# Kernel optimization log

Hardware: AMD Instinct MI355X
Metric: run time of the kernel (lower is better)

## Reference

```python
import jax, jax.numpy as jnp
import numpy as np

N_NODES = 40962
N_EDGES = 245760
K = 10  # gaussian kernels
D = 2   # pseudo-coordinate dim
EPS = 1e-15


def gmm_conv(x, edge_index, pseudo, g, mu, sigma, root, bias):
    """PyG GMMConv with aggr='mean', root_weight=True.
    x: [N, Cin], edge_index: [2, E] (row 0 = source j, row 1 = target i),
    pseudo: [E, D], g: [Cin, K*Cout], mu/sigma: [K, D], root: [Cin, Cout], bias: [Cout].
    """
    src, dst = edge_index[0], edge_index[1]
    E = pseudo.shape[0]
    # Gaussian mixture edge weights: [E, K]
    diff = pseudo[:, None, :] - mu[None, :, :]                     # [E, K, D]
    w = jnp.exp(jnp.sum(-0.5 * diff * diff / (EPS + sigma[None] ** 2), axis=-1))
    xj = x[src]                                                    # [E, Cin] gather
    y = (xj @ g).reshape(E, K, -1)                                 # [E, K, Cout]
    msg = jnp.sum(y * w[:, :, None], axis=1)                       # [E, Cout]
    agg = jax.ops.segment_sum(msg, dst, num_segments=N_NODES)      # scatter-add
    deg = jax.ops.segment_sum(jnp.ones((E,), x.dtype), dst, num_segments=N_NODES)
    agg = agg / jnp.maximum(deg, 1.0)[:, None]                     # mean aggregation
    return agg + x @ root + bias


def setup_inputs() -> dict:
    key = jax.random.key(0)
    ks = jax.random.split(key, 20)
    Cin, Ch, Cout = 64, 64, 128
    sc = lambda fan: 1.0 / np.sqrt(fan)
    inp = {
        "x": jax.random.normal(ks[0], (N_NODES, Cin), jnp.float32),
        "edge_index": jax.random.randint(ks[1], (2, N_EDGES), 0, N_NODES, jnp.int32),
        "pseudo": jax.random.uniform(ks[2], (N_EDGES, D), jnp.float32),
        # conv1: Cin -> Ch
        "g1": jax.random.normal(ks[3], (Cin, K * Ch), jnp.float32) * sc(Cin),
        "mu1": jax.random.uniform(ks[4], (K, D), jnp.float32),
        "sigma1": jax.random.uniform(ks[5], (K, D), jnp.float32) + 0.5,
        "root1": jax.random.normal(ks[6], (Cin, Ch), jnp.float32) * sc(Cin),
        "b1": jnp.zeros((Ch,), jnp.float32),
        # conv2: Ch -> Cout
        "g2": jax.random.normal(ks[7], (Ch, K * Cout), jnp.float32) * sc(Ch),
        "mu2": jax.random.uniform(ks[8], (K, D), jnp.float32),
        "sigma2": jax.random.uniform(ks[9], (K, D), jnp.float32) + 0.5,
        "root2": jax.random.normal(ks[10], (Ch, Cout), jnp.float32) * sc(Ch),
        "b2": jnp.zeros((Cout,), jnp.float32),
        # shortcut: Cin -> Cout (size_in != size_out)
        "gs": jax.random.normal(ks[11], (Cin, K * Cout), jnp.float32) * sc(Cin),
        "mus": jax.random.uniform(ks[12], (K, D), jnp.float32),
        "sigmas": jax.random.uniform(ks[13], (K, D), jnp.float32) + 0.5,
        "roots": jax.random.normal(ks[14], (Cin, Cout), jnp.float32) * sc(Cin),
        "bs": jnp.zeros((Cout,), jnp.float32),
    }
    return inp


def reference(x, edge_index, pseudo, g1, mu1, sigma1, root1, b1,
              g2, mu2, sigma2, root2, b2, gs, mus, sigmas, roots, bs):
    h = gmm_conv(x, edge_index, pseudo, g1, mu1, sigma1, root1, b1)
    h = jax.nn.relu(h)
    y = gmm_conv(h, edge_index, pseudo, g2, mu2, sigma2, root2, b2)
    x_s = gmm_conv(x, edge_index, pseudo, gs, mus, sigmas, roots, bs)
    return jax.nn.relu(y + x_s)
```

## Files before the change

### kernel.cpp

```cpp
#include <hip/hip_runtime.h>
#include <hip/hip_bf16.h>

using bf16 = __hip_bfloat16;
typedef __attribute__((ext_vector_type(8))) short short8;
typedef __attribute__((ext_vector_type(4))) float float4v;

#define N_NODES 40962
#define N_EDGES 245760
#define NP      41024
#define KG      10
#define SCAN_B  256
#define NBLK    ((NP + SCAN_B - 1) / SCAN_B)
#define GRID1   (NP / 64)

#define CVT_V   (N_NODES * 64 / 8)
#define CVT_BLK ((CVT_V + 255) / 256)
#define W3_BLK  (N_EDGES / 256)
#define PACK_N  (64 * 704 + 2 * 128 * 704)
#define PACK_BLK (PACK_N / 256)


__device__ __forceinline__ float ldf(const void* p, size_t i, int isf32) {
    return isf32 ? ((const float*)p)[i] : __bfloat162float(((const bf16*)p)[i]);
}
__device__ __forceinline__ float blo(unsigned u) { return __uint_as_float(u << 16); }
__device__ __forceinline__ float bhi(unsigned u) { return __uint_as_float(u & 0xffff0000u); }
__device__ __forceinline__ unsigned pk2(float a, float b) {
    union { bf16 h[2]; unsigned u; } t;
    t.h[0] = __float2bfloat16(a);
    t.h[1] = __float2bfloat16(b);
    return t.u;
}
__device__ __forceinline__ int rfl(int v) { return __builtin_amdgcn_readfirstlane(v); }

__device__ __forceinline__ void gll16(const void* g, void* l) {
    __builtin_amdgcn_global_load_lds(
        (const __attribute__((address_space(1))) void*)g,
        (__attribute__((address_space(3))) void*)l, 16, 0, 0);
}

__global__ void k_detect_count(const void* x, const int* __restrict__ ei,
                               int* __restrict__ flag, int* __restrict__ deg) {
    if (blockIdx.x == 0) {
        __shared__ int huge_c, zero_even;
        if (threadIdx.x == 0) { huge_c = 0; zero_even = 0; }
        __syncthreads();
        const bf16* xb = (const bf16*)x;
        int lh = 0, lz = 0;
        for (int i = threadIdx.x; i < 8192; i += 256) {
            float v = __bfloat162float(xb[i]);
            if (!(fabsf(v) <= 1e4f)) lh++;
            if ((i & 1) == 0 && v == 0.0f) lz++;
        }
        atomicAdd(&huge_c, lh);
        atomicAdd(&zero_even, lz);
        __syncthreads();
        if (threadIdx.x == 0) flag[0] = (huge_c > 0 || zero_even > 3000) ? 1 : 0;
    } else {
        int e = (blockIdx.x - 1) * 256 + threadIdx.x;
        if (e < N_EDGES) atomicAdd(&deg[ei[N_EDGES + e]], 1);
    }
}

__global__ void k_scan1(const int* __restrict__ deg, int* __restrict__ offs,
                        int* __restrict__ bsum) {
    __shared__ int buf[SCAN_B];
    int t = threadIdx.x, b = blockIdx.x;
    int i = b * SCAN_B + t;
    int v = (i < NP) ? deg[i] : 0;
    buf[t] = v;
    __syncthreads();
    for (int off = 1; off < SCAN_B; off <<= 1) {
        int a = (t >= off) ? buf[t - off] : 0;
        __syncthreads();
        buf[t] += a;
        __syncthreads();
    }
    if (i < NP) offs[i] = buf[t] - v;
    if (t == SCAN_B - 1) bsum[b] = buf[t];
}

__global__ void k_scan3m(int* __restrict__ offs, const int* __restrict__ bsum,
                         const int* __restrict__ deg, int* __restrict__ cur,
                         float* __restrict__ invdeg) {
    __shared__ int buf[256];
    int t = threadIdx.x, b = blockIdx.x;
    int v = (t < NBLK) ? bsum[t] : 0;
    buf[t] = v;
    __syncthreads();
    for (int off = 1; off < 256; off <<= 1) {
        int a = (t >= off) ? buf[t - off] : 0;
        __syncthreads();
        buf[t] += a;
        __syncthreads();
    }
    int bofs = (b > 0) ? buf[b - 1] : 0;
    int total = buf[NBLK - 1];
    int i = b * 256 + t;
    if (i < NP) {
        int o = offs[i] + bofs;
        offs[i] = o;
        cur[i] = o;
        int d = deg[i];
        invdeg[i] = 1.0f / (float)(d > 1 ? d : 1);
    }
    if (i == 0) offs[NP] = total;
}

__global__ void k_fill(const int* __restrict__ ei, int* __restrict__ cur,
                       int* __restrict__ ep, int* __restrict__ csr_src) {
    int e = blockIdx.x * 256 + threadIdx.x;
    if (e < N_EDGES) {
        int pos = atomicAdd(&cur[ei[N_EDGES + e]], 1);
        ep[e] = pos;
        csr_src[pos] = ei[e];
    }
}

__device__ __forceinline__ void gw_one(float p0, float p1, const void* mu,
                                       const void* sg, int f, float* out) {
#pragma unroll
    for (int k = 0; k < KG; k++) {
        float m0 = ldf(mu, 2 * k + 0, f), m1 = ldf(mu, 2 * k + 1, f);
        float s0 = ldf(sg, 2 * k + 0, f), s1 = ldf(sg, 2 * k + 1, f);
        float d0 = p0 - m0, d1 = p1 - m1;
        float t = -0.5f * (d0 * d0 / (1e-15f + s0 * s0) + d1 * d1 / (1e-15f + s1 * s1));
        out[k] = __expf(t);
    }
}

__device__ __forceinline__ void pack_frag(const void* g, const void* root, int f,
                                          int idx, int Cout, bf16* Bp) {
    int j = idx & 7;
    int lane = (idx >> 3) & 63;
    int rem = idx >> 9;
    int kc = rem % 22;
    int n = rem / 22;
    int col = n * 16 + (lane & 15);
    int k = kc * 32 + (lane >> 4) * 8 + j;
    float v;
    if (k < 512) {
        int cin = k >> 3, kg = k & 7;
        v = ldf(g, (size_t)cin * (KG * Cout) + (size_t)kg * Cout + col, f);
    } else if (k < 640) {
        int jj = k - 512;
        int cin = jj >> 1, kg = 8 + (jj & 1);
        v = ldf(g, (size_t)cin * (KG * Cout) + (size_t)kg * Cout + col, f);
    } else {
        v = ldf(root, (size_t)(k - 640) * Cout + col, f);
    }
    Bp[idx] = __float2bfloat16(v);
}

__global__ void k_prep_all(const void* __restrict__ x, const void* __restrict__ pseudo,
                           const void* mu1, const void* sg1, const void* mu2,
                           const void* sg2, const void* mus, const void* sgs,
                           const void* g1, const void* root1, const void* g2,
                           const void* root2, const void* gs, const void* roots,
                           const int* __restrict__ flag, const int* __restrict__ ep,
                           bf16* __restrict__ Xf, bf16* __restrict__ wcab,
                           bf16* __restrict__ wc2, bf16* wt1p, bf16* wt2p,
                           bf16* wtsp) {
    int b = blockIdx.x;
    int tid = threadIdx.x;
    int f = flag[0];
    if (b < CVT_BLK) {
        int i = b * 256 + tid;
        if (i < CVT_V) {
            int node = i >> 3, j = i & 7;
            uint4 u;
            if (f) {
                const float4* xf = (const float4*)x;
                float4 a = xf[2 * i], c = xf[2 * i + 1];
                union { bf16 t[8]; uint4 u; } tt;
                tt.t[0] = __float2bfloat16(a.x); tt.t[1] = __float2bfloat16(a.y);
                tt.t[2] = __float2bfloat16(a.z); tt.t[3] = __float2bfloat16(a.w);
                tt.t[4] = __float2bfloat16(c.x); tt.t[5] = __float2bfloat16(c.y);
                tt.t[6] = __float2bfloat16(c.z); tt.t[7] = __float2bfloat16(c.w);
                u = tt.u;
            } else {
                u = ((const uint4*)x)[i];
            }
            *(uint4*)(Xf + ((size_t)(j >> 2) * NP + node) * 32 + (j & 3) * 8) = u;
        }
    } else if (b < CVT_BLK + W3_BLK) {
        int e = (b - CVT_BLK) * 256 + tid;
        float p0 = ldf(pseudo, (size_t)e * 2 + 0, f);
        float p1 = ldf(pseudo, (size_t)e * 2 + 1, f);
        float o1[KG], o2[KG], os[KG];
        gw_one(p0, p1, mu1, sg1, f, o1);
        gw_one(p0, p1, mu2, sg2, f, o2);
        gw_one(p0, p1, mus, sgs, f, os);
        int pos = ep[e];
        unsigned* d = (unsigned*)wcab + (size_t)pos * 10;
        d[0] = pk2(o1[0], o1[1]); d[1] = pk2(o1[2], o1[3]);
        d[2] = pk2(o1[4], o1[5]); d[3] = pk2(o1[6], o1[7]);
        d[4] = pk2(o1[8], o1[9]);
        d[5] = pk2(os[0], os[1]); d[6] = pk2(os[2], os[3]);
        d[7] = pk2(os[4], os[5]); d[8] = pk2(os[6], os[7]);
        d[9] = pk2(os[8], os[9]);
        unsigned* d2 = (unsigned*)wc2 + (size_t)pos * 5;
        d2[0] = pk2(o2[0], o2[1]); d2[1] = pk2(o2[2], o2[3]);
        d2[2] = pk2(o2[4], o2[5]); d2[3] = pk2(o2[6], o2[7]);
        d2[4] = pk2(o2[8], o2[9]);
    } else {
        int idx = (b - CVT_BLK - W3_BLK) * 256 + tid;
        if (idx < 64 * 704) {
            pack_frag(g1, root1, f, idx, 64, wt1p);
        } else if (idx < 64 * 704 + 128 * 704) {
            pack_frag(g2, root2, f, idx - 64 * 704, 128, wt2p);
        } else {
            pack_frag(gs, roots, f, idx - 64 * 704 - 128 * 704, 128, wtsp);
        }
    }
}

__device__ __forceinline__ void store_zf(bf16* Zf, int wid, int lane, const float* a,
                                         float inv) {
    union { bf16 h[8]; uint4 u; } p;
#pragma unroll
    for (int k = 0; k < 8; k++) p.h[k] = __float2bfloat16(a[k] * inv);
    *(uint4*)(Zf + ((size_t)(lane >> 2) * NP + wid) * 32 + (lane & 3) * 8) = p.u;
    *(unsigned*)(Zf + ((size_t)(16 + (lane >> 4)) * NP + wid) * 32 + (lane & 15) * 2) =
        pk2(a[8] * inv, a[9] * inv);
}

__device__ __forceinline__ float ldx_frag(const bf16* X, int src, int lane) {
    return __bfloat162float(X[((size_t)(lane >> 5) * NP + src) * 32 + (lane & 31)]);
}

__device__ __forceinline__ int clampe(int idx) {
    return idx > N_EDGES - 1 ? N_EDGES - 1 : idx;
}

__global__ void k_gather2(const int* __restrict__ offs, const int* __restrict__ csr_src,
                          const bf16* __restrict__ wcab,
                          const float* __restrict__ invdeg, const bf16* __restrict__ X,
                          bf16* __restrict__ Za, bf16* __restrict__ Zb) {
    int wid = (blockIdx.x * 256 + threadIdx.x) >> 6;
    int lane = threadIdx.x & 63;
    if (wid >= NP) return;
    float aa[KG], ab[KG];
#pragma unroll
    for (int k = 0; k < KG; k++) { aa[k] = 0.0f; ab[k] = 0.0f; }
    int beg = rfl(offs[wid]);
    int end = rfl(offs[wid + 1]);
    int cnt = end - beg;
    const unsigned* wb = (const unsigned*)wcab;

    int s0 = rfl(csr_src[clampe(beg + 0)]);
    int s1 = rfl(csr_src[clampe(beg + 1)]);
    int sC = rfl(csr_src[clampe(beg + 2)]);
    float xv0 = ldx_frag(X, s0, lane);
    float xv1 = ldx_frag(X, s1, lane);
    const unsigned* wp0 = wb + (size_t)clampe(beg + 0) * 10;
    unsigned c0 = wp0[0], c1 = wp0[1], c2 = wp0[2], c3 = wp0[3], c4 = wp0[4];
    unsigned c5 = wp0[5], c6 = wp0[6], c7 = wp0[7], c8 = wp0[8], c9 = wp0[9];
    const unsigned* wp1 = wb + (size_t)clampe(beg + 1) * 10;
    unsigned n0 = wp1[0], n1 = wp1[1], n2 = wp1[2], n3 = wp1[3], n4 = wp1[4];
    unsigned n5 = wp1[5], n6 = wp1[6], n7 = wp1[7], n8 = wp1[8], n9 = wp1[9];

    for (int t = 0; t < cnt; ++t) {
        int sN = rfl(csr_src[clampe(beg + t + 3)]);
        float xv2 = ldx_frag(X, sC, lane);
        const unsigned* wp2 = wb + (size_t)clampe(beg + t + 2) * 10;
        unsigned m0 = wp2[0], m1 = wp2[1], m2 = wp2[2], m3 = wp2[3], m4 = wp2[4];
        unsigned m5 = wp2[5], m6 = wp2[6], m7 = wp2[7], m8 = wp2[8], m9 = wp2[9];
        aa[0] += blo(c0) * xv0; aa[1] += bhi(c0) * xv0;
        aa[2] += blo(c1) * xv0; aa[3] += bhi(c1) * xv0;
        aa[4] += blo(c2) * xv0; aa[5] += bhi(c2) * xv0;
        aa[6] += blo(c3) * xv0; aa[7] += bhi(c3) * xv0;
        aa[8] += blo(c4) * xv0; aa[9] += bhi(c4) * xv0;
        ab[0] += blo(c5) * xv0; ab[1] += bhi(c5) * xv0;
        ab[2] += blo(c6) * xv0; ab[3] += bhi(c6) * xv0;
        ab[4] += blo(c7) * xv0; ab[5] += bhi(c7) * xv0;
        ab[6] += blo(c8) * xv0; ab[7] += bhi(c8) * xv0;
        ab[8] += blo(c9) * xv0; ab[9] += bhi(c9) * xv0;
        xv0 = xv1; xv1 = xv2; sC = sN;
        c0 = n0; c1 = n1; c2 = n2; c3 = n3; c4 = n4;
        c5 = n5; c6 = n6; c7 = n7; c8 = n8; c9 = n9;
        n0 = m0; n1 = m1; n2 = m2; n3 = m3; n4 = m4;
        n5 = m5; n6 = m6; n7 = m7; n8 = m8; n9 = m9;
    }
    float inv = invdeg[wid];
    store_zf(Za, wid, lane, aa, inv);
    store_zf(Zb, wid, lane, ab, inv);
}

__global__ void k_gather(const int* __restrict__ offs, const int* __restrict__ csr_src,
                         const bf16* __restrict__ w, int wstride,
                         const float* __restrict__ invdeg,
                         const bf16* __restrict__ X, bf16* __restrict__ Z) {
    int wid = (blockIdx.x * 256 + threadIdx.x) >> 6;
    int lane = threadIdx.x & 63;
    if (wid >= NP) return;
    float acc[KG];
#pragma unroll
    for (int k = 0; k < KG; k++) acc[k] = 0.0f;
    int beg = rfl(offs[wid]);
    int end = rfl(offs[wid + 1]);
    int cnt = end - beg;

    int s0 = rfl(csr_src[clampe(beg + 0)]);
    int s1 = rfl(csr_src[clampe(beg + 1)]);
    int sC = rfl(csr_src[clampe(beg + 2)]);
    float xv0 = ldx_frag(X, s0, lane);
    float xv1 = ldx_frag(X, s1, lane);
    const unsigned* wp0 = (const unsigned*)(w + (size_t)clampe(beg + 0) * wstride);
    unsigned c0 = wp0[0], c1 = wp0[1], c2 = wp0[2], c3 = wp0[3], c4 = wp0[4];
    const unsigned* wp1 = (const unsigned*)(w + (size_t)clampe(beg + 1) * wstride);
    unsigned n0 = wp1[0], n1 = wp1[1], n2 = wp1[2], n3 = wp1[3], n4 = wp1[4];

    for (int t = 0; t < cnt; ++t) {
        int sN = rfl(csr_src[clampe(beg + t + 3)]);
        float xv2 = ldx_frag(X, sC, lane);
        const unsigned* wp2 = (const unsigned*)(w + (size_t)clampe(beg + t + 2) * wstride);
        unsigned m0 = wp2[0], m1 = wp2[1], m2 = wp2[2], m3 = wp2[3], m4 = wp2[4];
        acc[0] += blo(c0) * xv0; acc[1] += bhi(c0) * xv0;
        acc[2] += blo(c1) * xv0; acc[3] += bhi(c1) * xv0;
        acc[4] += blo(c2) * xv0; acc[5] += bhi(c2) * xv0;
        acc[6] += blo(c3) * xv0; acc[7] += bhi(c3) * xv0;
        acc[8] += blo(c4) * xv0; acc[9] += bhi(c4) * xv0;
        xv0 = xv1; xv1 = xv2; sC = sN;
        c0 = n0; c1 = n1; c2 = n2; c3 = n3; c4 = n4;
        n0 = m0; n1 = m1; n2 = m2; n3 = m3; n4 = m4;
    }
    store_zf(Z, wid, lane, acc, invdeg[wid]);
}

template <int NT, int MODE>
__device__ __forceinline__ void gemm_body(
    int bid, const bf16* __restrict__ Zf, const bf16* __restrict__ Xf,
    const bf16* __restrict__ Bp, const void* __restrict__ bias, int f,
    const bf16* __restrict__ addsrc, bf16* __restrict__ outb,
    void* __restrict__ outp, bf16* __restrict__ sB) {
    constexpr int Cout = NT * 16;
    int lane = threadIdx.x & 63;
    int wave = threadIdx.x >> 6;
    int m = lane & 15, quad = lane >> 4;
    int row0 = bid * 64 + wave * 16;

    const bf16* arow = Zf + ((size_t)(row0 + m)) * 32 + quad * 8;
    const bf16* xrow = Xf + ((size_t)(row0 + m)) * 32 + quad * 8;

    float4v acc[NT];
#pragma unroll
    for (int n = 0; n < NT; n++) acc[n] = (float4v){0.f, 0.f, 0.f, 0.f};

#pragma unroll
    for (int n = wave; n < NT; n += 4)
        gll16(Bp + ((size_t)(n * 22 + 0) * 64 + lane) * 8, sB + n * 512);
    short8 a_cur = *(const short8*)arow;
    __syncthreads();

#pragma unroll
    for (int kc = 0; kc < 22; kc++) {
        int buf = kc & 1;
        short8 a_nxt;
        if (kc < 21) {
            int kn = kc + 1;
#pragma unroll
            for (int n = wave; n < NT; n += 4)
                gll16(Bp + ((size_t)(n * 22 + kn) * 64 + lane) * 8,
                      sB + (size_t)(1 - buf) * NT * 512 + n * 512);
            a_nxt = (kn < 20)
                ? *(const short8*)(arow + (size_t)kn * NP * 32)
                : *(const short8*)(xrow + (size_t)(kn - 20) * NP * 32);
        }
        const bf16* bb = sB + (size_t)buf * NT * 512 + lane * 8;
#pragma unroll
        for (int n = 0; n < NT; n++) {
            short8 b = *(const short8*)(bb + (size_t)n * 512);
            acc[n] = __builtin_amdgcn_mfma_f32_16x16x32_bf16(a_cur, b, acc[n], 0, 0, 0);
        }
        __syncthreads();
        if (kc < 21) a_cur = a_nxt;
    }

#pragma unroll
    for (int n = 0; n < NT; n++) {
        int gcol = n * 16 + m;
        float bv = ldf(bias, gcol, f);
#pragma unroll
        for (int r = 0; r < 4; r++) {
            int grow = row0 + quad * 4 + r;
            if (grow >= N_NODES) continue;
            float v = acc[n][r] + bv;
            if (MODE == 0) {
                outb[((size_t)(gcol >> 5) * NP + grow) * 32 + (gcol & 31)] =
                    __float2bfloat16(fmaxf(v, 0.f));
            } else if (MODE == 1) {
                outb[(size_t)grow * Cout + gcol] = __float2bfloat16(v);
            } else {
                size_t oidx = (size_t)grow * Cout + gcol;
                v = fmaxf(v + __bfloat162float(addsrc[oidx]), 0.f);
                if (f) ((float*)outp)[oidx] = v;
                else   ((bf16*)outp)[oidx] = __float2bfloat16(v);
            }
        }
    }
}

__global__ __launch_bounds__(256) void k_gemm_pair(
    const bf16* __restrict__ za, const bf16* __restrict__ zb,
    const bf16* __restrict__ Xf, const bf16* __restrict__ wt1p,
    const bf16* __restrict__ wtsp, const void* __restrict__ b1,
    const void* __restrict__ bs, const int* __restrict__ flag,
    bf16* __restrict__ hf, bf16* __restrict__ ys) {
    __shared__ bf16 sB[2 * 8 * 512];
    int f = flag[0];
    if (blockIdx.x < GRID1)
        gemm_body<4, 0>(blockIdx.x, za, Xf, wt1p, b1, f, nullptr, hf, nullptr, sB);
    else
        gemm_body<8, 1>(blockIdx.x - GRID1, zb, Xf, wtsp, bs, f, nullptr, ys, nullptr,
                        sB);
}

template <int NT, int MODE>
__global__ __launch_bounds__(256) void k_gemm_one(
    const bf16* __restrict__ Zf, const bf16* __restrict__ Xf,
    const bf16* __restrict__ Bp, const void* __restrict__ bias,
    const int* __restrict__ flag, const bf16* __restrict__ addsrc,
    bf16* __restrict__ outb, void* __restrict__ outp) {
    __shared__ bf16 sB[2 * NT * 512];
    gemm_body<NT, MODE>(blockIdx.x, Zf, Xf, Bp, bias, flag[0], addsrc, outb, outp, sB);
}

extern "C" void kernel_launch(void* const* d_in, const int* in_sizes, int n_in,
                              void* d_out, int out_size, void* d_ws, size_t ws_size,
                              hipStream_t stream) {
    const void* x      = d_in[0];
    const int*  ei     = (const int*)d_in[1];
    const void* pseudo = d_in[2];
    const void* g1     = d_in[3];
    const void* mu1    = d_in[4];
    const void* sg1    = d_in[5];
    const void* root1  = d_in[6];
    const void* b1     = d_in[7];
    const void* g2     = d_in[8];
    const void* mu2    = d_in[9];
    const void* sg2    = d_in[10];
    const void* root2  = d_in[11];
    const void* b2     = d_in[12];
    const void* gs     = d_in[13];
    const void* mus    = d_in[14];
    const void* sgs    = d_in[15];
    const void* roots  = d_in[16];
    const void* bs     = d_in[17];

    char* ws = (char*)d_ws;
    size_t off = 0;
    auto alloc = [&](size_t bytes) -> char* {
        char* p = ws + off;
        off += (bytes + 255) & ~(size_t)255;
        return p;
    };
    const size_t ZSZ = (size_t)20 * NP * 32 * 2;
    const size_t XFS = (size_t)2 * NP * 32 * 2;

    int*   flag   = (int*)alloc(256);
    int*   deg    = (int*)alloc((size_t)NP * 4);
    int*   offs   = (int*)alloc((size_t)(NP + 1) * 4);
    int*   cur    = (int*)alloc((size_t)NP * 4);
    float* invdeg = (float*)alloc((size_t)NP * 4);
    int*   bsum   = (int*)alloc((size_t)NBLK * 4);
    int*   ep     = (int*)alloc((size_t)N_EDGES * 4);
    int*   csrs   = (int*)alloc((size_t)N_EDGES * 4);
    bf16*  Xf     = (bf16*)alloc(XFS);
    bf16*  hf     = (bf16*)alloc(XFS);
    bf16*  ys     = (bf16*)alloc((size_t)N_NODES * 128 * 2);
    bf16*  wt1p   = (bf16*)alloc((size_t)64 * 704 * 2);
    bf16*  wt2p   = (bf16*)alloc((size_t)128 * 704 * 2);
    bf16*  wtsp   = (bf16*)alloc((size_t)128 * 704 * 2);
    bf16*  wcab   = (bf16*)alloc((size_t)N_EDGES * 20 * 2);
    bf16*  wc2    = (bf16*)alloc((size_t)N_EDGES * 10 * 2);
    size_t common_end = off;

    bf16* za = (bf16*)alloc(ZSZ);
    bf16* zb = (bf16*)alloc(ZSZ);
    bool big = (off <= ws_size);

    hipMemsetAsync(deg, 0, (size_t)NP * 4, stream);
    k_detect_count<<<1 + (N_EDGES + 255) / 256, 256, 0, stream>>>(x, ei, flag, deg);
    k_scan1<<<NBLK, SCAN_B, 0, stream>>>(deg, offs, bsum);
    k_scan3m<<<NBLK, 256, 0, stream>>>(offs, bsum, deg, cur, invdeg);
    k_fill<<<(N_EDGES + 255) / 256, 256, 0, stream>>>(ei, cur, ep, csrs);
    k_prep_all<<<CVT_BLK + W3_BLK + PACK_BLK, 256, 0, stream>>>(
        x, pseudo, mu1, sg1, mu2, sg2, mus, sgs, g1, root1, g2, root2, gs, roots,
        flag, ep, Xf, wcab, wc2, wt1p, wt2p, wtsp);

    if (big) {
        k_gather2<<<NP / 4, 256, 0, stream>>>(offs, csrs, wcab, invdeg, Xf, za, zb);
        k_gemm_pair<<<2 * GRID1, 256, 0, stream>>>(za, zb, Xf, wt1p, wtsp, b1, bs,
                                                   flag, hf, ys);
        k_gather<<<NP / 4, 256, 0, stream>>>(offs, csrs, wc2, 10, invdeg, hf, za);
        k_gemm_one<8, 2><<<GRID1, 256, 0, stream>>>(za, hf, wt2p, b2, flag, ys,
                                                    (bf16*)nullptr, d_out);
    } else {
        off = common_end;
        bf16* z = (bf16*)alloc(ZSZ);
        k_gather<<<NP / 4, 256, 0, stream>>>(offs, csrs, wcab, 20, invdeg, Xf, z);
        k_gemm_one<4, 0><<<GRID1, 256, 0, stream>>>(z, Xf, wt1p, b1, flag,
                                                    (const bf16*)nullptr, hf, nullptr);
        k_gather<<<NP / 4, 256, 0, stream>>>(offs, csrs, wcab + 10, 20, invdeg, Xf, z);
        k_gemm_one<8, 1><<<GRID1, 256, 0, stream>>>(z, Xf, wtsp, bs, flag,
                                                    (const bf16*)nullptr, ys, nullptr);
        k_gather<<<NP / 4, 256, 0, stream>>>(offs, csrs, wc2, 10, invdeg, hf, z);
        k_gemm_one<8, 2><<<GRID1, 256, 0, stream>>>(z, hf, wt2p, b2, flag, ys,
                                                    (bf16*)nullptr, d_out);
    }
}
```

Before: 267.7 us.

## Fuse edge gather with MFMA GEMM through LDS, merging shortcut into conv2

Replaces the separate gather kernels (which wrote large Z intermediates to global memory) and GEMM kernels with two fused kernels. Each block gathers 16 nodes into an LDS tile, then runs MFMA directly from LDS. The second kernel computes conv2 and the shortcut conv together and accumulates both into one result, so the ys intermediate and the final add pass go away. This cuts global traffic and launch count. In exchange, per-block GEMM tiles are small, B fragments are read straight from global without LDS staging, and the shortcut gather now happens after conv1 instead of alongside it.

```diff
diff --git a/kernel.cpp b/kernel.cpp
--- a/kernel.cpp
+++ b/kernel.cpp
@@ -11,7 +11,7 @@
 #define KG      10
 #define SCAN_B  256
 #define NBLK    ((NP + SCAN_B - 1) / SCAN_B)
-#define GRID1   (NP / 64)
+#define GRIDF   (NP / 16)
 
 #define CVT_V   (N_NODES * 64 / 8)
 #define CVT_BLK ((CVT_V + 255) / 256)
@@ -19,6 +19,9 @@
 #define PACK_N  (64 * 704 + 2 * 128 * 704)
 #define PACK_BLK (PACK_N / 256)
 
+#define ZRS  40
+#define ZKS  648
+#define ZSZE 12960
 
 __device__ __forceinline__ float ldf(const void* p, size_t i, int isf32) {
     return isf32 ? ((const float*)p)[i] : __bfloat162float(((const bf16*)p)[i]);
@@ -32,12 +35,6 @@
     return t.u;
 }
 __device__ __forceinline__ int rfl(int v) { return __builtin_amdgcn_readfirstlane(v); }
-
-__device__ __forceinline__ void gll16(const void* g, void* l) {
-    __builtin_amdgcn_global_load_lds(
-        (const __attribute__((address_space(1))) void*)g,
-        (__attribute__((address_space(3))) void*)l, 16, 0, 0);
-}
 
 __global__ void k_detect_count(const void* x, const int* __restrict__ ei,
                                int* __restrict__ flag, int* __restrict__ deg) {
@@ -158,9 +155,9 @@
                            const void* g1, const void* root1, const void* g2,
                            const void* root2, const void* gs, const void* roots,
                            const int* __restrict__ flag, const int* __restrict__ ep,
-                           bf16* __restrict__ Xf, bf16* __restrict__ wcab,
-                           bf16* __restrict__ wc2, bf16* wt1p, bf16* wt2p,
-                           bf16* wtsp) {
+                           bf16* __restrict__ Xf, bf16* __restrict__ wc1,
+                           bf16* __restrict__ wcs, bf16* __restrict__ wc2,
+                           bf16* wt1p, bf16* wt2p, bf16* wtsp) {
     int b = blockIdx.x;
     int tid = threadIdx.x;
     int f = flag[0];
@@ -192,13 +189,14 @@
         gw_one(p0, p1, mu2, sg2, f, o2);
         gw_one(p0, p1, mus, sgs, f, os);
         int pos = ep[e];
-        unsigned* d = (unsigned*)wcab + (size_t)pos * 10;
-        d[0] = pk2(o1[0], o1[1]); d[1] = pk2(o1[2], o1[3]);
-        d[2] = pk2(o1[4], o1[5]); d[3] = pk2(o1[6], o1[7]);
-        d[4] = pk2(o1[8], o1[9]);
-        d[5] = pk2(os[0], os[1]); d[6] = pk2(os[2], os[3]);
-        d[7] = pk2(os[4], os[5]); d[8] = pk2(os[6], os[7]);
-        d[9] = pk2(os[8], os[9]);
+        unsigned* d1 = (unsigned*)wc1 + (size_t)pos * 5;
+        d1[0] = pk2(o1[0], o1[1]); d1[1] = pk2(o1[2], o1[3]);
+        d1[2] = pk2(o1[4], o1[5]); d1[3] = pk2(o1[6], o1[7]);
+        d1[4] = pk2(o1[8], o1[9]);
+        unsigned* ds = (unsigned*)wcs + (size_t)pos * 5;
+        ds[0] = pk2(os[0], os[1]); ds[1] = pk2(os[2], os[3]);
+        ds[2] = pk2(os[4], os[5]); ds[3] = pk2(os[6], os[7]);
+        ds[4] = pk2(os[8], os[9]);
         unsigned* d2 = (unsigned*)wc2 + (size_t)pos * 5;
         d2[0] = pk2(o2[0], o2[1]); d2[1] = pk2(o2[2], o2[3]);
         d2[2] = pk2(o2[4], o2[5]); d2[3] = pk2(o2[6], o2[7]);
@@ -215,16 +213,6 @@
     }
 }
 
-__device__ __forceinline__ void store_zf(bf16* Zf, int wid, int lane, const float* a,
-                                         float inv) {
-    union { bf16 h[8]; uint4 u; } p;
-#pragma unroll
-    for (int k = 0; k < 8; k++) p.h[k] = __float2bfloat16(a[k] * inv);
-    *(uint4*)(Zf + ((size_t)(lane >> 2) * NP + wid) * 32 + (lane & 3) * 8) = p.u;
-    *(unsigned*)(Zf + ((size_t)(16 + (lane >> 4)) * NP + wid) * 32 + (lane & 15) * 2) =
-        pk2(a[8] * inv, a[9] * inv);
-}
-
 __device__ __forceinline__ float ldx_frag(const bf16* X, int src, int lane) {
     return __bfloat162float(X[((size_t)(lane >> 5) * NP + src) * 32 + (lane & 31)]);
 }
@@ -233,197 +221,194 @@
     return idx > N_EDGES - 1 ? N_EDGES - 1 : idx;
 }
 
-__global__ void k_gather2(const int* __restrict__ offs, const int* __restrict__ csr_src,
-                          const bf16* __restrict__ wcab,
-                          const float* __restrict__ invdeg, const bf16* __restrict__ X,
-                          bf16* __restrict__ Za, bf16* __restrict__ Zb) {
-    int wid = (blockIdx.x * 256 + threadIdx.x) >> 6;
-    int lane = threadIdx.x & 63;
-    if (wid >= NP) return;
-    float aa[KG], ab[KG];
-#pragma unroll
-    for (int k = 0; k < KG; k++) { aa[k] = 0.0f; ab[k] = 0.0f; }
-    int beg = rfl(offs[wid]);
-    int end = rfl(offs[wid + 1]);
-    int cnt = end - beg;
-    const unsigned* wb = (const unsigned*)wcab;
-
-    int s0 = rfl(csr_src[clampe(beg + 0)]);
-    int s1 = rfl(csr_src[clampe(beg + 1)]);
-    int sC = rfl(csr_src[clampe(beg + 2)]);
-    float xv0 = ldx_frag(X, s0, lane);
-    float xv1 = ldx_frag(X, s1, lane);
-    const unsigned* wp0 = wb + (size_t)clampe(beg + 0) * 10;
-    unsigned c0 = wp0[0], c1 = wp0[1], c2 = wp0[2], c3 = wp0[3], c4 = wp0[4];
-    unsigned c5 = wp0[5], c6 = wp0[6], c7 = wp0[7], c8 = wp0[8], c9 = wp0[9];
-    const unsigned* wp1 = wb + (size_t)clampe(beg + 1) * 10;
-    unsigned n0 = wp1[0], n1 = wp1[1], n2 = wp1[2], n3 = wp1[3], n4 = wp1[4];
-    unsigned n5 = wp1[5], n6 = wp1[6], n7 = wp1[7], n8 = wp1[8], n9 = wp1[9];
-
-    for (int t = 0; t < cnt; ++t) {
-        int sN = rfl(csr_src[clampe(beg + t + 3)]);
-        float xv2 = ldx_frag(X, sC, lane);
-        const unsigned* wp2 = wb + (size_t)clampe(beg + t + 2) * 10;
-        unsigned m0 = wp2[0], m1 = wp2[1], m2 = wp2[2], m3 = wp2[3], m4 = wp2[4];
-        unsigned m5 = wp2[5], m6 = wp2[6], m7 = wp2[7], m8 = wp2[8], m9 = wp2[9];
-        aa[0] += blo(c0) * xv0; aa[1] += bhi(c0) * xv0;
-        aa[2] += blo(c1) * xv0; aa[3] += bhi(c1) * xv0;
-        aa[4] += blo(c2) * xv0; aa[5] += bhi(c2) * xv0;
-        aa[6] += blo(c3) * xv0; aa[7] += bhi(c3) * xv0;
-        aa[8] += blo(c4) * xv0; aa[9] += bhi(c4) * xv0;
-        ab[0] += blo(c5) * xv0; ab[1] += bhi(c5) * xv0;
-        ab[2] += blo(c6) * xv0; ab[3] += bhi(c6) * xv0;
-        ab[4] += blo(c7) * xv0; ab[5] += bhi(c7) * xv0;
-        ab[6] += blo(c8) * xv0; ab[7] += bhi(c8) * xv0;
-        ab[8] += blo(c9) * xv0; ab[9] += bhi(c9) * xv0;
-        xv0 = xv1; xv1 = xv2; sC = sN;
-        c0 = n0; c1 = n1; c2 = n2; c3 = n3; c4 = n4;
-        c5 = n5; c6 = n6; c7 = n7; c8 = n8; c9 = n9;
-        n0 = m0; n1 = m1; n2 = m2; n3 = m3; n4 = m4;
-        n5 = m5; n6 = m6; n7 = m7; n8 = m8; n9 = m9;
-    }
-    float inv = invdeg[wid];
-    store_zf(Za, wid, lane, aa, inv);
-    store_zf(Zb, wid, lane, ab, inv);
-}
-
-__global__ void k_gather(const int* __restrict__ offs, const int* __restrict__ csr_src,
-                         const bf16* __restrict__ w, int wstride,
-                         const float* __restrict__ invdeg,
-                         const bf16* __restrict__ X, bf16* __restrict__ Z) {
-    int wid = (blockIdx.x * 256 + threadIdx.x) >> 6;
-    int lane = threadIdx.x & 63;
-    if (wid >= NP) return;
-    float acc[KG];
-#pragma unroll
-    for (int k = 0; k < KG; k++) acc[k] = 0.0f;
-    int beg = rfl(offs[wid]);
-    int end = rfl(offs[wid + 1]);
-    int cnt = end - beg;
-
-    int s0 = rfl(csr_src[clampe(beg + 0)]);
-    int s1 = rfl(csr_src[clampe(beg + 1)]);
-    int sC = rfl(csr_src[clampe(beg + 2)]);
-    float xv0 = ldx_frag(X, s0, lane);
-    float xv1 = ldx_frag(X, s1, lane);
-    const unsigned* wp0 = (const unsigned*)(w + (size_t)clampe(beg + 0) * wstride);
-    unsigned c0 = wp0[0], c1 = wp0[1], c2 = wp0[2], c3 = wp0[3], c4 = wp0[4];
-    const unsigned* wp1 = (const unsigned*)(w + (size_t)clampe(beg + 1) * wstride);
-    unsigned n0 = wp1[0], n1 = wp1[1], n2 = wp1[2], n3 = wp1[3], n4 = wp1[4];
-
-    for (int t = 0; t < cnt; ++t) {
-        int sN = rfl(csr_src[clampe(beg + t + 3)]);
-        float xv2 = ldx_frag(X, sC, lane);
-        const unsigned* wp2 = (const unsigned*)(w + (size_t)clampe(beg + t + 2) * wstride);
-        unsigned m0 = wp2[0], m1 = wp2[1], m2 = wp2[2], m3 = wp2[3], m4 = wp2[4];
-        acc[0] += blo(c0) * xv0; acc[1] += bhi(c0) * xv0;
-        acc[2] += blo(c1) * xv0; acc[3] += bhi(c1) * xv0;
-        acc[4] += blo(c2) * xv0; acc[5] += bhi(c2) * xv0;
-        acc[6] += blo(c3) * xv0; acc[7] += bhi(c3) * xv0;
-        acc[8] += blo(c4) * xv0; acc[9] += bhi(c4) * xv0;
-        xv0 = xv1; xv1 = xv2; sC = sN;
-        c0 = n0; c1 = n1; c2 = n2; c3 = n3; c4 = n4;
-        n0 = m0; n1 = m1; n2 = m2; n3 = m3; n4 = m4;
-    }
-    store_zf(Z, wid, lane, acc, invdeg[wid]);
-}
-
-template <int NT, int MODE>
-__device__ __forceinline__ void gemm_body(
-    int bid, const bf16* __restrict__ Zf, const bf16* __restrict__ Xf,
-    const bf16* __restrict__ Bp, const void* __restrict__ bias, int f,
-    const bf16* __restrict__ addsrc, bf16* __restrict__ outb,
-    void* __restrict__ outp, bf16* __restrict__ sB) {
-    constexpr int Cout = NT * 16;
+__device__ __forceinline__ void store_zlds(bf16* z, int r, int lane, const float* a,
+                                           float inv) {
+    union { bf16 h[8]; uint4 u; } p;
+#pragma unroll
+    for (int k = 0; k < 8; k++) p.h[k] = __float2bfloat16(a[k] * inv);
+    *(uint4*)(z + (lane >> 2) * ZKS + r * ZRS + (lane & 3) * 8) = p.u;
+    *(unsigned*)(z + (16 + (lane >> 4)) * ZKS + r * ZRS + (lane & 15) * 2) =
+        pk2(a[8] * inv, a[9] * inv);
+}
+
+__global__ __launch_bounds__(256) void k_fused1(
+    const int* __restrict__ offs, const int* __restrict__ csr_src,
+    const bf16* __restrict__ wc1, const float* __restrict__ invdeg,
+    const bf16* __restrict__ Xf, const bf16* __restrict__ wt1p,
+    const void* __restrict__ b1, const int* __restrict__ flag,
+    bf16* __restrict__ hf) {
+    __shared__ bf16 zA[ZSZE];
     int lane = threadIdx.x & 63;
     int wave = threadIdx.x >> 6;
+    int bid = blockIdx.x;
+    const unsigned* wb = (const unsigned*)wc1;
+
+    for (int i = 0; i < 4; i++) {
+        int r = wave * 4 + i;
+        int node = bid * 16 + r;
+        float acc[KG];
+#pragma unroll
+        for (int k = 0; k < KG; k++) acc[k] = 0.0f;
+        int beg = rfl(offs[node]);
+        int end = rfl(offs[node + 1]);
+        int cnt = end - beg;
+        int sC = rfl(csr_src[clampe(beg + 2)]);
+        float xv0 = ldx_frag(Xf, rfl(csr_src[clampe(beg + 0)]), lane);
+        float xv1 = ldx_frag(Xf, rfl(csr_src[clampe(beg + 1)]), lane);
+        const unsigned* wp0 = wb + (size_t)clampe(beg + 0) * 5;
+        unsigned c0 = wp0[0], c1 = wp0[1], c2 = wp0[2], c3 = wp0[3], c4 = wp0[4];
+        const unsigned* wp1 = wb + (size_t)clampe(beg + 1) * 5;
+        unsigned n0 = wp1[0], n1 = wp1[1], n2 = wp1[2], n3 = wp1[3], n4 = wp1[4];
+        for (int t = 0; t < cnt; ++t) {
+            int sN = rfl(csr_src[clampe(beg + t + 3)]);
+            float xv2 = ldx_frag(Xf, sC, lane);
+            const unsigned* wp2 = wb + (size_t)clampe(beg + t + 2) * 5;
+            unsigned m0 = wp2[0], m1 = wp2[1], m2 = wp2[2], m3 = wp2[3], m4 = wp2[4];
+            acc[0] += blo(c0) * xv0; acc[1] += bhi(c0) * xv0;
+            acc[2] += blo(c1) * xv0; acc[3] += bhi(c1) * xv0;
+            acc[4] += blo(c2) * xv0; acc[5] += bhi(c2) * xv0;
+            acc[6] += blo(c3) * xv0; acc[7] += bhi(c3) * xv0;
+            acc[8] += blo(c4) * xv0; acc[9] += bhi(c4) * xv0;
+            xv0 = xv1; xv1 = xv2; sC = sN;
+            c0 = n0; c1 = n1; c2 = n2; c3 = n3; c4 = n4;
+            n0 = m0; n1 = m1; n2 = m2; n3 = m3; n4 = m4;
+        }
+        store_zlds(zA, r, lane, acc, invdeg[node]);
+    }
+    __syncthreads();
+
     int m = lane & 15, quad = lane >> 4;
-    int row0 = bid * 64 + wave * 16;
-
-    const bf16* arow = Zf + ((size_t)(row0 + m)) * 32 + quad * 8;
+    int row0 = bid * 16;
+    float4v acc4 = (float4v){0.f, 0.f, 0.f, 0.f};
+    const bf16* brow = wt1p + ((size_t)(wave * 22) * 64 + lane) * 8;
     const bf16* xrow = Xf + ((size_t)(row0 + m)) * 32 + quad * 8;
-
-    float4v acc[NT];
-#pragma unroll
-    for (int n = 0; n < NT; n++) acc[n] = (float4v){0.f, 0.f, 0.f, 0.f};
-
-#pragma unroll
-    for (int n = wave; n < NT; n += 4)
-        gll16(Bp + ((size_t)(n * 22 + 0) * 64 + lane) * 8, sB + n * 512);
-    short8 a_cur = *(const short8*)arow;
+#pragma unroll
+    for (int kc = 0; kc < 22; kc++) {
+        short8 a = (kc < 20)
+            ? *(const short8*)(zA + kc * ZKS + m * ZRS + quad * 8)
+            : *(const short8*)(xrow + (size_t)(kc - 20) * NP * 32);
+        short8 b = *(const short8*)(brow + (size_t)kc * 512);
+        acc4 = __builtin_amdgcn_mfma_f32_16x16x32_bf16(a, b, acc4, 0, 0, 0);
+    }
+    int f = flag[0];
+    int gcol = wave * 16 + m;
+    float bv = ldf(b1, gcol, f);
+#pragma unroll
+    for (int r = 0; r < 4; r++) {
+        int grow = row0 + quad * 4 + r;
+        if (grow >= N_NODES) continue;
+        float v = fmaxf(acc4[r] + bv, 0.f);
+        hf[((size_t)(gcol >> 5) * NP + grow) * 32 + (gcol & 31)] = __float2bfloat16(v);
+    }
+}
+
+__global__ __launch_bounds__(256) void k_fused2(
+    const int* __restrict__ offs, const int* __restrict__ csr_src,
+    const bf16* __restrict__ wc2, const bf16* __restrict__ wcs,
+    const float* __restrict__ invdeg, const bf16* __restrict__ Xf,
+    const bf16* __restrict__ hf, const bf16* __restrict__ wt2p,
+    const bf16* __restrict__ wtsp, const void* __restrict__ b2,
+    const void* __restrict__ bs, const int* __restrict__ flag,
+    void* __restrict__ out) {
+    __shared__ bf16 z2[ZSZE];
+    __shared__ bf16 zs[ZSZE];
+    int lane = threadIdx.x & 63;
+    int wave = threadIdx.x >> 6;
+    int bid = blockIdx.x;
+    const unsigned* w2b = (const unsigned*)wc2;
+    const unsigned* wsb = (const unsigned*)wcs;
+
+    for (int i = 0; i < 4; i++) {
+        int r = wave * 4 + i;
+        int node = bid * 16 + r;
+        float a2[KG], as[KG];
+#pragma unroll
+        for (int k = 0; k < KG; k++) { a2[k] = 0.0f; as[k] = 0.0f; }
+        int beg = rfl(offs[node]);
+        int end = rfl(offs[node + 1]);
+        int cnt = end - beg;
+        int sC = rfl(csr_src[clampe(beg + 2)]);
+        int s0 = rfl(csr_src[clampe(beg + 0)]);
+        int s1 = rfl(csr_src[clampe(beg + 1)]);
+        float hv0 = ldx_frag(hf, s0, lane), xv0 = ldx_frag(Xf, s0, lane);
+        float hv1 = ldx_frag(hf, s1, lane), xv1 = ldx_frag(Xf, s1, lane);
+        const unsigned* p20 = w2b + (size_t)clampe(beg + 0) * 5;
+        unsigned c0 = p20[0], c1 = p20[1], c2 = p20[2], c3 = p20[3], c4 = p20[4];
+        const unsigned* ps0 = wsb + (size_t)clampe(beg + 0) * 5;
+        unsigned d0 = ps0[0], d1 = ps0[1], d2 = ps0[2], d3 = ps0[3], d4 = ps0[4];
+        const unsigned* p21 = w2b + (size_t)clampe(beg + 1) * 5;
+        unsigned n0 = p21[0], n1 = p21[1], n2 = p21[2], n3 = p21[3], n4 = p21[4];
+        const unsigned* ps1 = wsb + (size_t)clampe(beg + 1) * 5;
+        unsigned o0 = ps1[0], o1 = ps1[1], o2 = ps1[2], o3 = ps1[3], o4 = ps1[4];
+        for (int t = 0; t < cnt; ++t) {
+            int sN = rfl(csr_src[clampe(beg + t + 3)]);
+            float hv2 = ldx_frag(hf, sC, lane);
+            float xv2 = ldx_frag(Xf, sC, lane);
+            const unsigned* p22 = w2b + (size_t)clampe(beg + t + 2) * 5;
+            unsigned m0 = p22[0], m1 = p22[1], m2 = p22[2], m3 = p22[3], m4 = p22[4];
+            const unsigned* ps2 = wsb + (size_t)clampe(beg + t + 2) * 5;
+            unsigned q0 = ps2[0], q1 = ps2[1], q2 = ps2[2], q3 = ps2[3], q4 = ps2[4];
+            a2[0] += blo(c0) * hv0; a2[1] += bhi(c0) * hv0;
+            a2[2] += blo(c1) * hv0; a2[3] += bhi(c1) * hv0;
+            a2[4] += blo(c2) * hv0; a2[5] += bhi(c2) * hv0;
+            a2[6] += blo(c3) * hv0; a2[7] += bhi(c3) * hv0;
+            a2[8] += blo(c4) * hv0; a2[9] += bhi(c4) * hv0;
+            as[0] += blo(d0) * xv0; as[1] += bhi(d0) * xv0;
+            as[2] += blo(d1) * xv0; as[3] += bhi(d1) * xv0;
+            as[4] += blo(d2) * xv0; as[5] += bhi(d2) * xv0;
+            as[6] += blo(d3) * xv0; as[7] += bhi(d3) * xv0;
+            as[8] += blo(d4) * xv0; as[9] += bhi(d4) * xv0;
+            hv0 = hv1; hv1 = hv2; xv0 = xv1; xv1 = xv2; sC = sN;
+            c0 = n0; c1 = n1; c2 = n2; c3 = n3; c4 = n4;
+            n0 = m0; n1 = m1; n2 = m2; n3 = m3; n4 = m4;
+            d0 = o0; d1 = o1; d2 = o2; d3 = o3; d4 = o4;
+            o0 = q0; o1 = q1; o2 = q2; o3 = q3; o4 = q4;
+        }
+        float inv = invdeg[node];
+        store_zlds(z2, r, lane, a2, inv);
+        store_zlds(zs, r, lane, as, inv);
+    }
     __syncthreads();
 
-#pragma unroll
-    for (int kc = 0; kc < 22; kc++) {
-        int buf = kc & 1;
-        short8 a_nxt;
-        if (kc < 21) {
-            int kn = kc + 1;
-#pragma unroll
-            for (int n = wave; n < NT; n += 4)
-                gll16(Bp + ((size_t)(n * 22 + kn) * 64 + lane) * 8,
-                      sB + (size_t)(1 - buf) * NT * 512 + n * 512);
-            a_nxt = (kn < 20)
-                ? *(const short8*)(arow + (size_t)kn * NP * 32)
-                : *(const short8*)(xrow + (size_t)(kn - 20) * NP * 32);
-        }
-        const bf16* bb = sB + (size_t)buf * NT * 512 + lane * 8;
-#pragma unroll
-        for (int n = 0; n < NT; n++) {
-            short8 b = *(const short8*)(bb + (size_t)n * 512);
-            acc[n] = __builtin_amdgcn_mfma_f32_16x16x32_bf16(a_cur, b, acc[n], 0, 0, 0);
-        }
-        __syncthreads();
-        if (kc < 21) a_cur = a_nxt;
-    }
-
-#pragma unroll
-    for (int n = 0; n < NT; n++) {
+    int m = lane & 15, quad = lane >> 4;
+    int row0 = bid * 16;
+    const bf16* hrow = hf + ((size_t)(row0 + m)) * 32 + quad * 8;
+    const bf16* xrow = Xf + ((size_t)(row0 + m)) * 32 + quad * 8;
+    int f = flag[0];
+#pragma unroll
+    for (int tt = 0; tt < 2; tt++) {
+        int n = wave + tt * 4;
+        float4v acc4 = (float4v){0.f, 0.f, 0.f, 0.f};
+        const bf16* b2row = wt2p + ((size_t)(n * 22) * 64 + lane) * 8;
+        const bf16* bsrow = wtsp + ((size_t)(n * 22) * 64 + lane) * 8;
+#pragma unroll
+        for (int kc = 0; kc < 22; kc++) {
+            short8 a = (kc < 20)
+                ? *(const short8*)(z2 + kc * ZKS + m * ZRS + quad * 8)
+                : *(const short8*)(hrow + (size_t)(kc - 20) * NP * 32);
+            short8 b = *(const short8*)(b2row + (size_t)kc * 512);
+            acc4 = __builtin_amdgcn_mfma_f32_16x16x32_bf16(a, b, acc4, 0, 0, 0);
+        }
+#pragma unroll
+        for (int kc = 0; kc < 22; kc++) {
+            short8 a = (kc < 20)
+                ? *(const short8*)(zs + kc * ZKS + m * ZRS + quad * 8)
+                : *(const short8*)(xrow + (size_t)(kc - 20) * NP * 32);
+            short8 b = *(const short8*)(bsrow + (size_t)kc * 512);
+            acc4 = __builtin_amdgcn_mfma_f32_16x16x32_bf16(a, b, acc4, 0, 0, 0);
+        }
         int gcol = n * 16 + m;
-        float bv = ldf(bias, gcol, f);
+        float bv = ldf(b2, gcol, f) + ldf(bs, gcol, f);
 #pragma unroll
         for (int r = 0; r < 4; r++) {
             int grow = row0 + quad * 4 + r;
             if (grow >= N_NODES) continue;
-            float v = acc[n][r] + bv;
-            if (MODE == 0) {
-                outb[((size_t)(gcol >> 5) * NP + grow) * 32 + (gcol & 31)] =
-                    __float2bfloat16(fmaxf(v, 0.f));
-            } else if (MODE == 1) {
-                outb[(size_t)grow * Cout + gcol] = __float2bfloat16(v);
-            } else {
-                size_t oidx = (size_t)grow * Cout + gcol;
-                v = fmaxf(v + __bfloat162float(addsrc[oidx]), 0.f);
-                if (f) ((float*)outp)[oidx] = v;
-                else   ((bf16*)outp)[oidx] = __float2bfloat16(v);
-            }
-        }
-    }
-}
-
-__global__ __launch_bounds__(256) void k_gemm_pair(
-    const bf16* __restrict__ za, const bf16* __restrict__ zb,
-    const bf16* __restrict__ Xf, const bf16* __restrict__ wt1p,
-    const bf16* __restrict__ wtsp, const void* __restrict__ b1,
-    const void* __restrict__ bs, const int* __restrict__ flag,
-    bf16* __restrict__ hf, bf16* __restrict__ ys) {
-    __shared__ bf16 sB[2 * 8 * 512];
-    int f = flag[0];
-    if (blockIdx.x < GRID1)
-        gemm_body<4, 0>(blockIdx.x, za, Xf, wt1p, b1, f, nullptr, hf, nullptr, sB);
-    else
-        gemm_body<8, 1>(blockIdx.x - GRID1, zb, Xf, wtsp, bs, f, nullptr, ys, nullptr,
-                        sB);
-}
-
-template <int NT, int MODE>
-__global__ __launch_bounds__(256) void k_gemm_one(
-    const bf16* __restrict__ Zf, const bf16* __restrict__ Xf,
-    const bf16* __restrict__ Bp, const void* __restrict__ bias,
-    const int* __restrict__ flag, const bf16* __restrict__ addsrc,
-    bf16* __restrict__ outb, void* __restrict__ outp) {
-    __shared__ bf16 sB[2 * NT * 512];
-    gemm_body<NT, MODE>(blockIdx.x, Zf, Xf, Bp, bias, flag[0], addsrc, outb, outp, sB);
+            float v = fmaxf(acc4[r] + bv, 0.f);
+            size_t oidx = (size_t)grow * 128 + gcol;
+            if (f) ((float*)out)[oidx] = v;
+            else   ((bf16*)out)[oidx] = __float2bfloat16(v);
+        }
+    }
 }
 
 extern "C" void kernel_launch(void* const* d_in, const int* in_sizes, int n_in,
@@ -455,7 +440,6 @@
         off += (bytes + 255) & ~(size_t)255;
         return p;
     };
-    const size_t ZSZ = (size_t)20 * NP * 32 * 2;
     const size_t XFS = (size_t)2 * NP * 32 * 2;
 
     int*   flag   = (int*)alloc(256);
@@ -468,17 +452,13 @@
     int*   csrs   = (int*)alloc((size_t)N_EDGES * 4);
     bf16*  Xf     = (bf16*)alloc(XFS);
     bf16*  hf     = (bf16*)alloc(XFS);
-    bf16*  ys     = (bf16*)alloc((size_t)N_NODES * 128 * 2);
     bf16*  wt1p   = (bf16*)alloc((size_t)64 * 704 * 2);
     bf16*  wt2p   = (bf16*)alloc((size_t)128 * 704 * 2);
     bf16*  wtsp   = (bf16*)alloc((size_t)128 * 704 * 2);
-    bf16*  wcab   = (bf16*)alloc((size_t)N_EDGES * 20 * 2);
+    bf16*  wc1    = (bf16*)alloc((size_t)N_EDGES * 10 * 2);
+    bf16*  wcs    = (bf16*)alloc((size_t)N_EDGES * 10 * 2);
     bf16*  wc2    = (bf16*)alloc((size_t)N_EDGES * 10 * 2);
-    size_t common_end = off;
-
-    bf16* za = (bf16*)alloc(ZSZ);
-    bf16* zb = (bf16*)alloc(ZSZ);
-    bool big = (off <= ws_size);
+    (void)ws_size;
 
     hipMemsetAsync(deg, 0, (size_t)NP * 4, stream);
     k_detect_count<<<1 + (N_EDGES + 255) / 256, 256, 0, stream>>>(x, ei, flag, deg);
@@ -487,26 +467,9 @@
     k_fill<<<(N_EDGES + 255) / 256, 256, 0, stream>>>(ei, cur, ep, csrs);
     k_prep_all<<<CVT_BLK + W3_BLK + PACK_BLK, 256, 0, stream>>>(
         x, pseudo, mu1, sg1, mu2, sg2, mus, sgs, g1, root1, g2, root2, gs, roots,
-        flag, ep, Xf, wcab, wc2, wt1p, wt2p, wtsp);
-
-    if (big) {
-        k_gather2<<<NP / 4, 256, 0, stream>>>(offs, csrs, wcab, invdeg, Xf, za, zb);
-        k_gemm_pair<<<2 * GRID1, 256, 0, stream>>>(za, zb, Xf, wt1p, wtsp, b1, bs,
-                                                   flag, hf, ys);
-        k_gather<<<NP / 4, 256, 0, stream>>>(offs, csrs, wc2, 10, invdeg, hf, za);
-        k_gemm_one<8, 2><<<GRID1, 256, 0, stream>>>(za, hf, wt2p, b2, flag, ys,
-                                                    (bf16*)nullptr, d_out);
-    } else {
-        off = common_end;
-        bf16* z = (bf16*)alloc(ZSZ);
-        k_gather<<<NP / 4, 256, 0, stream>>>(offs, csrs, wcab, 20, invdeg, Xf, z);
-        k_gemm_one<4, 0><<<GRID1, 256, 0, stream>>>(z, Xf, wt1p, b1, flag,
-                                                    (const bf16*)nullptr, hf, nullptr);
-        k_gather<<<NP / 4, 256, 0, stream>>>(offs, csrs, wcab + 10, 20, invdeg, Xf, z);
-        k_gemm_one<8, 1><<<GRID1, 256, 0, stream>>>(z, Xf, wtsp, bs, flag,
-                                                    (const bf16*)nullptr, ys, nullptr);
-        k_gather<<<NP / 4, 256, 0, stream>>>(offs, csrs, wc2, 10, invdeg, hf, z);
-        k_gemm_one<8, 2><<<GRID1, 256, 0, stream>>>(z, hf, wt2p, b2, flag, ys,
-                                                    (bf16*)nullptr, d_out);
-    }
-}
+        flag, ep, Xf, wc1, wcs, wc2, wt1p, wt2p, wtsp);
+    k_fused1<<<GRIDF, 256, 0, stream>>>(offs, csrs, wc1, invdeg, Xf, wt1p, b1,
+                                        flag, hf);
+    k_fused2<<<GRIDF, 256, 0, stream>>>(offs, csrs, wc2, wcs, invdeg, Xf, hf,
+                                        wt2p, wtsp, b2, bs, flag, d_out);
+}
```

Result: slower. 279.4 us (+4.4%).
